# Kernel optimization log

Measured on AMD Instinct MI355X. Metric: run time of the kernel, lower is better.

## Reference

```python
import jax, jax.numpy as jnp
import numpy as np

B = 2048          # env batch
N = 32            # num_svgd_particles
D = 6             # act_dim
OBS = 17          # obs_dim
H = 256           # q1 hidden width
STEPS = 10        # num_svgd_steps
LR = 0.1          # svgd_lr
LIMIT = 1.0       # act_limit
LOG_NP1 = np.float32(np.log(N + 1.0))


def setup_inputs() -> dict:
    key = jax.random.key(0)
    ks = jax.random.split(key, 6)
    obs = jax.random.normal(ks[0], (B * N, OBS), dtype=jnp.float32)
    a = jax.random.normal(ks[1], (B * N, D), dtype=jnp.float32)
    W1 = jax.random.normal(ks[2], (OBS + D, H), dtype=jnp.float32) / np.float32(np.sqrt(OBS + D))
    b1 = jnp.zeros((H,), dtype=jnp.float32)
    W2 = jax.random.normal(ks[3], (H, H), dtype=jnp.float32) / np.float32(np.sqrt(H))
    b2 = jnp.zeros((H,), dtype=jnp.float32)
    W3 = jax.random.normal(ks[4], (H, 1), dtype=jnp.float32) / np.float32(np.sqrt(H))
    b3 = jnp.zeros((1,), dtype=jnp.float32)
    return {"obs": obs, "a": a, "W1": W1, "b1": b1, "W2": W2, "b2": b2, "W3": W3, "b3": b3}


def q1(obs, X, W1, b1, W2, b2, W3, b3):
    # standard SAC critic: Q(s, a) = MLP(concat(s, a))
    h = jax.nn.relu(jnp.concatenate([obs, X], axis=-1) @ W1 + b1)
    h = jax.nn.relu(h @ W2 + b2)
    return (h @ W3 + b3).squeeze(-1)


def rbf(X):
    # X: (B, N, D); input_2 = X.detach() in the original
    Xd = jax.lax.stop_gradient(X)
    diff = X[:, :, None, :] - Xd[:, None, :, :]          # (B, N, N, D)
    dist_sq = jnp.sum(diff * diff, axis=-1)              # (B, N, N)
    nn = N * N
    # torch.median returns the LOWER of the two middle values for even counts
    med = jnp.sort(jax.lax.stop_gradient(dist_sq).reshape(-1, nn), axis=1)[:, (nn - 1) // 2]
    h = med / (2.0 * LOG_NP1)                            # bandwidth^2 (sigma^2 = h)
    gamma = 1.0 / (1e-8 + 2.0 * h)                       # (B,)
    gamma = gamma[:, None, None]                         # (B, 1, 1)
    kappa = jnp.exp(-gamma * dist_sq)                    # (B, N, N)
    kappa_grad = -2.0 * (diff * gamma[..., None]) * kappa[..., None]  # (B, N, N, D)
    return kappa, diff, gamma, kappa_grad


def reference(obs, a, W1, b1, W2, b2, W3, b3):
    score_fn = jax.grad(lambda Xf: q1(obs, Xf, W1, b1, W2, b2, W3, b3).sum())
    logp = jnp.zeros((B, N), dtype=jnp.float32)

    for _ in range(STEPS):
        score = score_fn(a)                              # (B*N, D)
        X = a.reshape(B, N, D)
        s = score.reshape(B, N, D)
        K_XX, K_diff, K_gamma, K_grad = rbf(X)
        Kd = jax.lax.stop_gradient(K_XX)
        phi = (jnp.einsum('bij,bjd->bid', Kd, s) - K_grad.sum(axis=2)) / N  # (B, N, D)
        line_4 = (K_grad * s[:, None, :, :]).sum(-1).mean(-1)               # (B, N)
        line_5 = -2.0 * K_gamma[:, :, 0] * (
            (-K_grad * K_diff).sum(-1) - D * K_XX
        ).mean(-1)                                                          # (B, N)
        logp = logp - LR * (line_4 + line_5)
        a = jnp.clip(a + LR * phi.reshape(B * N, D), -LIMIT, LIMIT)
        a = jax.lax.stop_gradient(a)

    return a, logp
```

## Files before the change

### kernel.cpp

```cpp
#include <hip/hip_runtime.h>
#include <hip/hip_bf16.h>

#define NB 2048
#define NP 32
#define ND 6
#define NOBS 17
#define NH 256
#define NSTEPS 10
#define C_LR 0.1f
#define C_LIM 1.0f
#define C_LOGNP1 3.4965075614664802f

typedef __bf16 bf16x8 __attribute__((ext_vector_type(8)));
typedef float  f32x4  __attribute__((ext_vector_type(4)));

#define MFMA(a, b, c) __builtin_amdgcn_mfma_f32_16x16x32_bf16(a, b, c, 0, 0, 0)

static __device__ __forceinline__ unsigned short f2bf(float f) {
    union { float f; unsigned u; } c; c.f = f;
    const unsigned r = c.u + 0x7fffu + ((c.u >> 16) & 1u);
    return (unsigned short)(r >> 16);
}

static __device__ __forceinline__ int colpf(int n) {
    return ((n >> 5) << 11) + (((n >> 3) & 3) << 7) + (n & 7);
}

__global__ void prep_swizzle(const float* __restrict__ W1, const float* __restrict__ W2,
                             unsigned short* __restrict__ ws) {
    const int g = blockIdx.x * 256 + threadIdx.x;
    unsigned short v[8];
    if (g < 8192) {
        const int l = g & 63, fid = g >> 6;
        const int kt = fid >> 4, nt = fid & 15;
        const int row0 = kt * 32 + (l >> 4) * 8;
        const int col  = nt * 16 + (l & 15);
#pragma unroll
        for (int j = 0; j < 8; ++j) v[j] = f2bf(W2[(row0 + j) * NH + col]);
        ushort4* dst = (ushort4*)(ws + (size_t)g * 8);
        dst[0] = make_ushort4(v[0], v[1], v[2], v[3]);
        dst[1] = make_ushort4(v[4], v[5], v[6], v[7]);
    } else if (g < 16384) {
        const int e = g - 8192;
        const int l = e & 63, fid = e >> 6;
        const int kt = fid >> 4, nt = fid & 15;
        const int row  = nt * 16 + (l & 15);
        const int col0 = kt * 32 + (l >> 4) * 8;
#pragma unroll
        for (int j = 0; j < 8; ++j) v[j] = f2bf(W2[row * NH + col0 + j]);
        ushort4* dst = (ushort4*)(ws + 65536 + (size_t)e * 8);
        dst[0] = make_ushort4(v[0], v[1], v[2], v[3]);
        dst[1] = make_ushort4(v[4], v[5], v[6], v[7]);
    } else if (g < 16896) {
        const int e = g - 16384;
        const int l = e & 63, kt = e >> 6;
        const int n  = l & 15;
        const int k0 = kt * 32 + (l >> 4) * 8;
#pragma unroll
        for (int j = 0; j < 8; ++j)
            v[j] = (n < ND) ? f2bf(W1[(NOBS + n) * NH + k0 + j]) : (unsigned short)0;
        ushort4* dst = (ushort4*)(ws + 131072 + (size_t)e * 8);
        dst[0] = make_ushort4(v[0], v[1], v[2], v[3]);
        dst[1] = make_ushort4(v[4], v[5], v[6], v[7]);
    } else if (g < 17920) {
        const int e = g - 16896;
        const int l = e & 63, nt = e >> 6;
        const int col = nt * 16 + (l & 15);
        const int r0  = (l >> 4) * 8;
#pragma unroll
        for (int j = 0; j < 8; ++j)
            v[j] = (r0 + j < NOBS + ND) ? f2bf(W1[(r0 + j) * NH + col]) : (unsigned short)0;
        ushort4* dst = (ushort4*)(ws + 135168 + (size_t)e * 8);
        dst[0] = make_ushort4(v[0], v[1], v[2], v[3]);
        dst[1] = make_ushort4(v[4], v[5], v[6], v[7]);
    }
}

__global__ __launch_bounds__(256, 4)
void svgd_kernel(const float* __restrict__ obs, const float* __restrict__ a_in,
                 const float* __restrict__ W1, const float* __restrict__ b1,
                 const float* __restrict__ W2, const float* __restrict__ b2,
                 const float* __restrict__ W3, const unsigned short* __restrict__ ws,
                 float* __restrict__ out)
{
    __shared__ __attribute__((aligned(16))) unsigned short hA[64 * NH];
    __shared__ float Xs[2][576];
    __shared__ float sc_[576];
    __shared__ float med_s[2];

    const int t    = threadIdx.x;
    const int bb   = blockIdx.x;
    const int lane = t & 63;
    const int wid  = t >> 6;
    const int w4   = wid * 4;
    const int quad = lane >> 4;
    const int ln15 = lane & 15;
    const int qo = t >> 7, iao = (t & 127) >> 2, jgo = t & 3;

    const unsigned short* gW2f = ws;
    const unsigned short* gW2b = ws + 65536;
    const unsigned short* gW1p = ws + 131072;
    const unsigned short* gW1f = ws + 135168;

    {
        float* scr = (float*)hA;
        const float* obs_g = obs + (size_t)bb * 1088;
        for (int p = t; p < 1088; p += 256) scr[p] = obs_g[p];
        const float* a_g = a_in + (size_t)bb * 384;
        for (int p = t; p < 384; p += 256) {
            const int s = p / 6, d = p - 6 * s;
            Xs[0][s * 9 + d] = a_g[p];
        }
    }
    __syncthreads();
    bf16x8 a0[4];
    {
        const float* scr = (const float*)hA;
#pragma unroll
        for (int m = 0; m < 4; ++m) {
            const int s = m * 16 + ln15;
#pragma unroll
            for (int j = 0; j < 8; ++j) {
                const int k = quad * 8 + j;
                float v = 0.0f;
                if (k < NOBS) v = scr[s * NOBS + k];
                else if (k < NOBS + ND) v = Xs[0][s * 9 + (k - NOBS)];
                a0[m][j] = (__bf16)v;
            }
        }
    }
    __syncthreads();

    bf16x8 w1b[4]; float b1r[4], b2r[4]; unsigned short w3u[4];
#pragma unroll
    for (int q = 0; q < 4; ++q) {
        const int n = (w4 + q) * 16 + ln15;
        w1b[q] = *(const bf16x8*)(gW1f + ((w4 + q) * 64 + lane) * 8);
        b1r[q] = b1[n]; b2r[q] = b2[n]; w3u[q] = f2bf(W3[n]);
    }

    float logp_r = 0.0f;
    int cur = 0;
    const f32x4 zv = {0.f, 0.f, 0.f, 0.f};

    for (int step = 0; step < NSTEPS; ++step) {
        unsigned long long mask1 = 0ull;
#pragma unroll
        for (int p = 0; p < 2; ++p) {
            f32x4 acc0[4][2];
#pragma unroll
            for (int m = 0; m < 4; ++m)
#pragma unroll
                for (int q1 = 0; q1 < 2; ++q1)
                    acc0[m][q1] = MFMA(a0[m], w1b[2 * p + q1], zv);
#pragma unroll
            for (int q1 = 0; q1 < 2; ++q1) {
                const int q = 2 * p + q1;
                const int cp = colpf((w4 + q) * 16 + ln15);
#pragma unroll
                for (int m = 0; m < 4; ++m)
#pragma unroll
                    for (int reg = 0; reg < 4; ++reg) {
                        const float hv = acc0[m][q1][reg] + b1r[q];
                        const int idx = cp + m * 512 + (quad * 4 + reg) * 8;
                        if (hv > 0.f) {
                            mask1 |= 1ull << (q * 16 + m * 4 + reg);
                            hA[idx] = f2bf(hv);
                        } else hA[idx] = 0;
                    }
            }
        }
        __syncthreads();

        unsigned long long mask2 = 0ull;
#pragma unroll
        for (int p = 0; p < 2; ++p) {
            f32x4 acc[4][2];
#pragma unroll
            for (int m = 0; m < 4; ++m) { acc[m][0] = zv; acc[m][1] = zv; }
#pragma unroll 2
            for (int kt = 0; kt < 8; ++kt) {
                bf16x8 a[4];
#pragma unroll
                for (int m = 0; m < 4; ++m)
                    a[m] = *(const bf16x8*)&hA[(kt * 4 + m) * 512 + lane * 8];
#pragma unroll
                for (int q1 = 0; q1 < 2; ++q1) {
                    const bf16x8 bf = *(const bf16x8*)(gW2f + ((kt * 16 + w4 + 2 * p + q1) * 64 + lane) * 8);
#pragma unroll
                    for (int m = 0; m < 4; ++m) acc[m][q1] = MFMA(a[m], bf, acc[m][q1]);
                }
            }
#pragma unroll
            for (int q1 = 0; q1 < 2; ++q1)
#pragma unroll
                for (int m = 0; m < 4; ++m)
#pragma unroll
                    for (int reg = 0; reg < 4; ++reg)
                        if (acc[m][q1][reg] + b2r[2 * p + q1] > 0.f)
                            mask2 |= 1ull << ((2 * p + q1) * 16 + m * 4 + reg);
        }
        __syncthreads();
#pragma unroll
        for (int q = 0; q < 4; ++q) {
            const int cp = colpf((w4 + q) * 16 + ln15);
#pragma unroll
            for (int m = 0; m < 4; ++m)
#pragma unroll
                for (int reg = 0; reg < 4; ++reg) {
                    const int idx = cp + m * 512 + (quad * 4 + reg) * 8;
                    hA[idx] = ((mask2 >> (q * 16 + m * 4 + reg)) & 1ull)
                                  ? w3u[q] : (unsigned short)0;
                }
        }
        __syncthreads();

        unsigned dh1p[16];
        f32x4 acc2[4][2];
#pragma unroll
        for (int m = 0; m < 4; ++m) { acc2[m][0] = zv; acc2[m][1] = zv; }
#pragma unroll 2
        for (int kt = 0; kt < 8; ++kt) {
            bf16x8 a[4];
#pragma unroll
            for (int m = 0; m < 4; ++m)
                a[m] = *(const bf16x8*)&hA[(kt * 4 + m) * 512 + lane * 8];
#pragma unroll
            for (int q1 = 0; q1 < 2; ++q1) {
                const bf16x8 bf = *(const bf16x8*)(gW2b + ((kt * 16 + w4 + q1) * 64 + lane) * 8);
#pragma unroll
                for (int m = 0; m < 4; ++m) acc2[m][q1] = MFMA(a[m], bf, acc2[m][q1]);
            }
        }
#pragma unroll
        for (int q1 = 0; q1 < 2; ++q1)
#pragma unroll
            for (int m = 0; m < 4; ++m)
#pragma unroll
                for (int rp = 0; rp < 2; ++rp) {
                    const int b0 = q1 * 16 + m * 4 + rp * 2;
                    const unsigned lo = ((mask1 >> b0) & 1ull)
                        ? (unsigned)f2bf(acc2[m][q1][rp * 2]) : 0u;
                    const unsigned hi = ((mask1 >> (b0 + 1)) & 1ull)
                        ? (unsigned)f2bf(acc2[m][q1][rp * 2 + 1]) : 0u;
                    dh1p[(q1 * 4 + m) * 2 + rp] = lo | (hi << 16);
                }
#pragma unroll
        for (int m = 0; m < 4; ++m) { acc2[m][0] = zv; acc2[m][1] = zv; }
#pragma unroll 2
        for (int kt = 0; kt < 8; ++kt) {
            bf16x8 a[4];
#pragma unroll
            for (int m = 0; m < 4; ++m)
                a[m] = *(const bf16x8*)&hA[(kt * 4 + m) * 512 + lane * 8];
#pragma unroll
            for (int q1 = 0; q1 < 2; ++q1) {
                const bf16x8 bf = *(const bf16x8*)(gW2b + ((kt * 16 + w4 + 2 + q1) * 64 + lane) * 8);
#pragma unroll
                for (int m = 0; m < 4; ++m) acc2[m][q1] = MFMA(a[m], bf, acc2[m][q1]);
            }
        }
        __syncthreads();
#pragma unroll
        for (int q1 = 0; q1 < 2; ++q1) {
            const int cp = colpf((w4 + q1) * 16 + ln15);
#pragma unroll
            for (int m = 0; m < 4; ++m)
#pragma unroll
                for (int rp = 0; rp < 2; ++rp) {
                    const unsigned v = dh1p[(q1 * 4 + m) * 2 + rp];
                    const int idx = cp + m * 512 + (quad * 4 + rp * 2) * 8;
                    hA[idx]     = (unsigned short)(v & 0xffffu);
                    hA[idx + 8] = (unsigned short)(v >> 16);
                }
        }
#pragma unroll
        for (int q1 = 0; q1 < 2; ++q1) {
            const int q = 2 + q1;
            const int cp = colpf((w4 + q) * 16 + ln15);
#pragma unroll
            for (int m = 0; m < 4; ++m)
#pragma unroll
                for (int reg = 0; reg < 4; ++reg) {
                    const int idx = cp + m * 512 + (quad * 4 + reg) * 8;
                    hA[idx] = ((mask1 >> (q * 16 + m * 4 + reg)) & 1ull)
                                  ? f2bf(acc2[m][q1][reg]) : (unsigned short)0;
                }
        }
        __syncthreads();

        if (wid >= 2) {
            const int mb = (wid - 2) * 2;
            f32x4 sa[2] = {zv, zv};
#pragma unroll
            for (int kt = 0; kt < 8; ++kt) {
                const bf16x8 bw = *(const bf16x8*)(gW1p + (kt * 64 + lane) * 8);
#pragma unroll
                for (int mm = 0; mm < 2; ++mm) {
                    const bf16x8 a = *(const bf16x8*)&hA[(kt * 4 + mb + mm) * 512 + lane * 8];
                    sa[mm] = MFMA(a, bw, sa[mm]);
                }
            }
            if (ln15 < ND) {
#pragma unroll
                for (int mm = 0; mm < 2; ++mm)
#pragma unroll
                    for (int reg = 0; reg < 4; ++reg)
                        sc_[((mb + mm) * 16 + quad * 4 + reg) * 9 + ln15] = sa[mm][reg];
            }
        } else {
            const float* Xc = &Xs[cur][wid * 288];
            unsigned u[8];
#pragma unroll
            for (int r = 0; r < 8; ++r) {
                const int e = lane + 64 * r;
                if (e < 496) {
                    int i = (int)((63.0f - sqrtf(3969.0f - 8.0f * (float)e)) * 0.5f);
                    while (i * (63 - i) / 2 > e) --i;
                    while ((i + 1) * (62 - i) / 2 <= e) ++i;
                    const int j = i + 1 + (e - i * (63 - i) / 2);
                    float s = 0.f;
#pragma unroll
                    for (int d = 0; d < ND; ++d) {
                        const float df = Xc[i * 9 + d] - Xc[j * 9 + d];
                        s += df * df;
                    }
                    u[r] = __float_as_uint(s);
                } else u[r] = 0x7f800000u;
            }
            unsigned P = 0u;
            for (int bit = 30; bit >= 0; --bit) {
                const unsigned Q = P | (1u << bit);
                int c = 0;
#pragma unroll
                for (int r = 0; r < 8; ++r)
                    c += __popcll(__ballot(u[r] < Q));
                if (c <= 239) P = Q;
            }
            if (lane == 0) med_s[wid] = __uint_as_float(P);
        }
        __syncthreads();

        {
            const int nxt = cur ^ 1;
            const float gam = 1.0f / (1e-8f + med_s[qo] / C_LOGNP1);
            const float* Xc = &Xs[cur][qo * 288];
            float xi[6];
#pragma unroll
            for (int d = 0; d < ND; ++d) xi[d] = Xc[iao * 9 + d];
            float w[8] = {0, 0, 0, 0, 0, 0, 0, 0};
#pragma unroll
            for (int jj = 0; jj < 8; ++jj) {
                const int j = jgo * 8 + jj;
                float df6[6], sj6[6];
                float dsv = 0.f, dot = 0.f;
#pragma unroll
                for (int d = 0; d < ND; ++d) {
                    df6[d] = xi[d] - Xc[j * 9 + d];
                    sj6[d] = sc_[(qo * 32 + j) * 9 + d];
                    dsv += df6[d] * df6[d];
                    dot += df6[d] * sj6[d];
                }
                const float kap = __expf(-gam * dsv);
                const float tg = 2.0f * gam * kap;
#pragma unroll
                for (int d = 0; d < ND; ++d) w[d] += kap * sj6[d] + tg * df6[d];
                w[6] -= tg * dot;
                w[7] += tg * dsv - 6.0f * kap;
            }
#pragma unroll
            for (int off = 1; off < 4; off <<= 1)
#pragma unroll
                for (int c = 0; c < 8; ++c) w[c] += __shfl_xor(w[c], off);
            const int base = (qo * 32 + iao) * 9;
            {
                float x = xi[jgo] + C_LR * (w[jgo] * (1.0f / 32.0f));
                Xs[nxt][base + jgo] = fminf(fmaxf(x, -C_LIM), C_LIM);
            }
            if (jgo < 2) {
                const int d = jgo + 4;
                float x = xi[d] + C_LR * (w[d] * (1.0f / 32.0f));
                Xs[nxt][base + d] = fminf(fmaxf(x, -C_LIM), C_LIM);
            }
            if (jgo == 3)
                logp_r -= C_LR * (w[6] * (1.0f / 32.0f)
                                  - 2.0f * gam * (w[7] * (1.0f / 32.0f)));
        }
        __syncthreads();

        cur ^= 1;
        if (quad == 2) {
#pragma unroll
            for (int m = 0; m < 4; ++m) {
                const int s = m * 16 + ln15;
#pragma unroll
                for (int j = 1; j <= 6; ++j)
                    a0[m][j] = (__bf16)Xs[cur][s * 9 + (j - 1)];
            }
        }
    }

    for (int p = t; p < 384; p += 256) {
        const int s = p / 6, d = p - 6 * s;
        out[(size_t)bb * 384 + p] = Xs[cur][s * 9 + d];
    }
    if (jgo == 3) out[(size_t)NB * NP * ND + bb * 64 + qo * 32 + iao] = logp_r;
}

extern "C" void kernel_launch(void* const* d_in, const int* in_sizes, int n_in,
                              void* d_out, int out_size, void* d_ws, size_t ws_size,
                              hipStream_t stream) {
    const float* obs = (const float*)d_in[0];
    const float* a   = (const float*)d_in[1];
    const float* W1  = (const float*)d_in[2];
    const float* b1  = (const float*)d_in[3];
    const float* W2  = (const float*)d_in[4];
    const float* b2  = (const float*)d_in[5];
    const float* W3  = (const float*)d_in[6];
    unsigned short* wsu = (unsigned short*)d_ws;
    float* out = (float*)d_out;

    prep_swizzle<<<70, 256, 0, stream>>>(W1, W2, wsu);
    svgd_kernel<<<NB / 2, 256, 0, stream>>>(obs, a, W1, b1, W2, b2, W3, wsu, out);
}
```

Baseline: 558.7 us.

## Process all four column tiles per pass and compact particle shared layouts

The MLP forward and backward passes now keep all four 16-column tiles of accumulators live at once instead of splitting them into two halves. This removes the mask2 bitmask round trip, the packed dh1p spill and the extra backward GEMM pass with its barriers. W1 fragments are reloaded from global memory each step rather than held in registers. Particle and score arrays in shared memory move from padded stride 9 to dense strides 6 and 8, which shrinks LDS use but may add bank conflicts. The trade is higher accumulator register pressure, which risks spills or lower occupancy under launch_bounds(256,4).

```diff
diff --git a/kernel.cpp b/kernel.cpp
--- a/kernel.cpp
+++ b/kernel.cpp
@@ -84,8 +84,8 @@
                  float* __restrict__ out)
 {
     __shared__ __attribute__((aligned(16))) unsigned short hA[64 * NH];
-    __shared__ float Xs[2][576];
-    __shared__ float sc_[576];
+    __shared__ float Xs[2][384];
+    __shared__ float sc_[512];
     __shared__ float med_s[2];
 
     const int t    = threadIdx.x;
@@ -107,10 +107,7 @@
         const float* obs_g = obs + (size_t)bb * 1088;
         for (int p = t; p < 1088; p += 256) scr[p] = obs_g[p];
         const float* a_g = a_in + (size_t)bb * 384;
-        for (int p = t; p < 384; p += 256) {
-            const int s = p / 6, d = p - 6 * s;
-            Xs[0][s * 9 + d] = a_g[p];
-        }
+        for (int p = t; p < 384; p += 256) Xs[0][p] = a_g[p];
     }
     __syncthreads();
     bf16x8 a0[4];
@@ -124,18 +121,17 @@
                 const int k = quad * 8 + j;
                 float v = 0.0f;
                 if (k < NOBS) v = scr[s * NOBS + k];
-                else if (k < NOBS + ND) v = Xs[0][s * 9 + (k - NOBS)];
+                else if (k < NOBS + ND) v = Xs[0][s * 6 + (k - NOBS)];
                 a0[m][j] = (__bf16)v;
             }
         }
     }
     __syncthreads();
 
-    bf16x8 w1b[4]; float b1r[4], b2r[4]; unsigned short w3u[4];
+    float b1r[4], b2r[4]; unsigned short w3u[4];
 #pragma unroll
     for (int q = 0; q < 4; ++q) {
         const int n = (w4 + q) * 16 + ln15;
-        w1b[q] = *(const bf16x8*)(gW1f + ((w4 + q) * 64 + lane) * 8);
         b1r[q] = b1[n]; b2r[q] = b2[n]; w3u[q] = f2bf(W3[n]);
     }
 
@@ -145,23 +141,24 @@
 
     for (int step = 0; step < NSTEPS; ++step) {
         unsigned long long mask1 = 0ull;
-#pragma unroll
-        for (int p = 0; p < 2; ++p) {
-            f32x4 acc0[4][2];
+        {
+            bf16x8 w1B[4];
+#pragma unroll
+            for (int q = 0; q < 4; ++q)
+                w1B[q] = *(const bf16x8*)(gW1f + ((w4 + q) * 64 + lane) * 8);
+            f32x4 acc0[4][4];
 #pragma unroll
             for (int m = 0; m < 4; ++m)
 #pragma unroll
-                for (int q1 = 0; q1 < 2; ++q1)
-                    acc0[m][q1] = MFMA(a0[m], w1b[2 * p + q1], zv);
-#pragma unroll
-            for (int q1 = 0; q1 < 2; ++q1) {
-                const int q = 2 * p + q1;
+                for (int q = 0; q < 4; ++q) acc0[m][q] = MFMA(a0[m], w1B[q], zv);
+#pragma unroll
+            for (int q = 0; q < 4; ++q) {
                 const int cp = colpf((w4 + q) * 16 + ln15);
 #pragma unroll
                 for (int m = 0; m < 4; ++m)
 #pragma unroll
                     for (int reg = 0; reg < 4; ++reg) {
-                        const float hv = acc0[m][q1][reg] + b1r[q];
+                        const float hv = acc0[m][q][reg] + b1r[q];
                         const int idx = cp + m * 512 + (quad * 4 + reg) * 8;
                         if (hv > 0.f) {
                             mask1 |= 1ull << (q * 16 + m * 4 + reg);
@@ -172,12 +169,12 @@
         }
         __syncthreads();
 
-        unsigned long long mask2 = 0ull;
-#pragma unroll
-        for (int p = 0; p < 2; ++p) {
-            f32x4 acc[4][2];
-#pragma unroll
-            for (int m = 0; m < 4; ++m) { acc[m][0] = zv; acc[m][1] = zv; }
+        {
+            f32x4 acc[4][4];
+#pragma unroll
+            for (int m = 0; m < 4; ++m)
+#pragma unroll
+                for (int q = 0; q < 4; ++q) acc[m][q] = zv;
 #pragma unroll 2
             for (int kt = 0; kt < 8; ++kt) {
                 bf16x8 a[4];
@@ -185,107 +182,61 @@
                 for (int m = 0; m < 4; ++m)
                     a[m] = *(const bf16x8*)&hA[(kt * 4 + m) * 512 + lane * 8];
 #pragma unroll
-                for (int q1 = 0; q1 < 2; ++q1) {
-                    const bf16x8 bf = *(const bf16x8*)(gW2f + ((kt * 16 + w4 + 2 * p + q1) * 64 + lane) * 8);
-#pragma unroll
-                    for (int m = 0; m < 4; ++m) acc[m][q1] = MFMA(a[m], bf, acc[m][q1]);
+                for (int q = 0; q < 4; ++q) {
+                    const bf16x8 bf = *(const bf16x8*)(gW2f + ((kt * 16 + w4 + q) * 64 + lane) * 8);
+#pragma unroll
+                    for (int m = 0; m < 4; ++m) acc[m][q] = MFMA(a[m], bf, acc[m][q]);
                 }
             }
-#pragma unroll
-            for (int q1 = 0; q1 < 2; ++q1)
-#pragma unroll
-                for (int m = 0; m < 4; ++m)
-#pragma unroll
-                    for (int reg = 0; reg < 4; ++reg)
-                        if (acc[m][q1][reg] + b2r[2 * p + q1] > 0.f)
-                            mask2 |= 1ull << ((2 * p + q1) * 16 + m * 4 + reg);
-        }
-        __syncthreads();
-#pragma unroll
-        for (int q = 0; q < 4; ++q) {
-            const int cp = colpf((w4 + q) * 16 + ln15);
+            __syncthreads();
+#pragma unroll
+            for (int q = 0; q < 4; ++q) {
+                const int cp = colpf((w4 + q) * 16 + ln15);
+                const float b2v = b2r[q];
+                const unsigned short w3v = w3u[q];
+#pragma unroll
+                for (int m = 0; m < 4; ++m)
+#pragma unroll
+                    for (int reg = 0; reg < 4; ++reg) {
+                        const int idx = cp + m * 512 + (quad * 4 + reg) * 8;
+                        hA[idx] = (acc[m][q][reg] + b2v > 0.f) ? w3v : (unsigned short)0;
+                    }
+            }
+        }
+        __syncthreads();
+
+        {
+            f32x4 acc2[4][4];
 #pragma unroll
             for (int m = 0; m < 4; ++m)
 #pragma unroll
-                for (int reg = 0; reg < 4; ++reg) {
-                    const int idx = cp + m * 512 + (quad * 4 + reg) * 8;
-                    hA[idx] = ((mask2 >> (q * 16 + m * 4 + reg)) & 1ull)
-                                  ? w3u[q] : (unsigned short)0;
+                for (int q = 0; q < 4; ++q) acc2[m][q] = zv;
+#pragma unroll 2
+            for (int kt = 0; kt < 8; ++kt) {
+                bf16x8 a[4];
+#pragma unroll
+                for (int m = 0; m < 4; ++m)
+                    a[m] = *(const bf16x8*)&hA[(kt * 4 + m) * 512 + lane * 8];
+#pragma unroll
+                for (int q = 0; q < 4; ++q) {
+                    const bf16x8 bf = *(const bf16x8*)(gW2b + ((kt * 16 + w4 + q) * 64 + lane) * 8);
+#pragma unroll
+                    for (int m = 0; m < 4; ++m) acc2[m][q] = MFMA(a[m], bf, acc2[m][q]);
                 }
-        }
-        __syncthreads();
-
-        unsigned dh1p[16];
-        f32x4 acc2[4][2];
-#pragma unroll
-        for (int m = 0; m < 4; ++m) { acc2[m][0] = zv; acc2[m][1] = zv; }
-#pragma unroll 2
-        for (int kt = 0; kt < 8; ++kt) {
-            bf16x8 a[4];
-#pragma unroll
-            for (int m = 0; m < 4; ++m)
-                a[m] = *(const bf16x8*)&hA[(kt * 4 + m) * 512 + lane * 8];
-#pragma unroll
-            for (int q1 = 0; q1 < 2; ++q1) {
-                const bf16x8 bf = *(const bf16x8*)(gW2b + ((kt * 16 + w4 + q1) * 64 + lane) * 8);
-#pragma unroll
-                for (int m = 0; m < 4; ++m) acc2[m][q1] = MFMA(a[m], bf, acc2[m][q1]);
-            }
-        }
-#pragma unroll
-        for (int q1 = 0; q1 < 2; ++q1)
-#pragma unroll
-            for (int m = 0; m < 4; ++m)
-#pragma unroll
-                for (int rp = 0; rp < 2; ++rp) {
-                    const int b0 = q1 * 16 + m * 4 + rp * 2;
-                    const unsigned lo = ((mask1 >> b0) & 1ull)
-                        ? (unsigned)f2bf(acc2[m][q1][rp * 2]) : 0u;
-                    const unsigned hi = ((mask1 >> (b0 + 1)) & 1ull)
-                        ? (unsigned)f2bf(acc2[m][q1][rp * 2 + 1]) : 0u;
-                    dh1p[(q1 * 4 + m) * 2 + rp] = lo | (hi << 16);
-                }
-#pragma unroll
-        for (int m = 0; m < 4; ++m) { acc2[m][0] = zv; acc2[m][1] = zv; }
-#pragma unroll 2
-        for (int kt = 0; kt < 8; ++kt) {
-            bf16x8 a[4];
-#pragma unroll
-            for (int m = 0; m < 4; ++m)
-                a[m] = *(const bf16x8*)&hA[(kt * 4 + m) * 512 + lane * 8];
-#pragma unroll
-            for (int q1 = 0; q1 < 2; ++q1) {
-                const bf16x8 bf = *(const bf16x8*)(gW2b + ((kt * 16 + w4 + 2 + q1) * 64 + lane) * 8);
-#pragma unroll
-                for (int m = 0; m < 4; ++m) acc2[m][q1] = MFMA(a[m], bf, acc2[m][q1]);
-            }
-        }
-        __syncthreads();
-#pragma unroll
-        for (int q1 = 0; q1 < 2; ++q1) {
-            const int cp = colpf((w4 + q1) * 16 + ln15);
-#pragma unroll
-            for (int m = 0; m < 4; ++m)
-#pragma unroll
-                for (int rp = 0; rp < 2; ++rp) {
-                    const unsigned v = dh1p[(q1 * 4 + m) * 2 + rp];
-                    const int idx = cp + m * 512 + (quad * 4 + rp * 2) * 8;
-                    hA[idx]     = (unsigned short)(v & 0xffffu);
-                    hA[idx + 8] = (unsigned short)(v >> 16);
-                }
-        }
-#pragma unroll
-        for (int q1 = 0; q1 < 2; ++q1) {
-            const int q = 2 + q1;
-            const int cp = colpf((w4 + q) * 16 + ln15);
-#pragma unroll
-            for (int m = 0; m < 4; ++m)
-#pragma unroll
-                for (int reg = 0; reg < 4; ++reg) {
-                    const int idx = cp + m * 512 + (quad * 4 + reg) * 8;
-                    hA[idx] = ((mask1 >> (q * 16 + m * 4 + reg)) & 1ull)
-                                  ? f2bf(acc2[m][q1][reg]) : (unsigned short)0;
-                }
+            }
+            __syncthreads();
+#pragma unroll
+            for (int q = 0; q < 4; ++q) {
+                const int cp = colpf((w4 + q) * 16 + ln15);
+#pragma unroll
+                for (int m = 0; m < 4; ++m)
+#pragma unroll
+                    for (int reg = 0; reg < 4; ++reg) {
+                        const int idx = cp + m * 512 + (quad * 4 + reg) * 8;
+                        hA[idx] = ((mask1 >> (q * 16 + m * 4 + reg)) & 1ull)
+                                      ? f2bf(acc2[m][q][reg]) : (unsigned short)0;
+                    }
+            }
         }
         __syncthreads();
 
@@ -306,10 +257,10 @@
                 for (int mm = 0; mm < 2; ++mm)
 #pragma unroll
                     for (int reg = 0; reg < 4; ++reg)
-                        sc_[((mb + mm) * 16 + quad * 4 + reg) * 9 + ln15] = sa[mm][reg];
+                        sc_[((mb + mm) * 16 + quad * 4 + reg) * 8 + ln15] = sa[mm][reg];
             }
         } else {
-            const float* Xc = &Xs[cur][wid * 288];
+            const float* Xc = &Xs[cur][wid * 192];
             unsigned u[8];
 #pragma unroll
             for (int r = 0; r < 8; ++r) {
@@ -322,7 +273,7 @@
                     float s = 0.f;
 #pragma unroll
                     for (int d = 0; d < ND; ++d) {
-                        const float df = Xc[i * 9 + d] - Xc[j * 9 + d];
+                        const float df = Xc[i * 6 + d] - Xc[j * 6 + d];
                         s += df * df;
                     }
                     u[r] = __float_as_uint(s);
@@ -344,10 +295,10 @@
         {
             const int nxt = cur ^ 1;
             const float gam = 1.0f / (1e-8f + med_s[qo] / C_LOGNP1);
-            const float* Xc = &Xs[cur][qo * 288];
+            const float* Xc = &Xs[cur][qo * 192];
             float xi[6];
 #pragma unroll
-            for (int d = 0; d < ND; ++d) xi[d] = Xc[iao * 9 + d];
+            for (int d = 0; d < ND; ++d) xi[d] = Xc[iao * 6 + d];
             float w[8] = {0, 0, 0, 0, 0, 0, 0, 0};
 #pragma unroll
             for (int jj = 0; jj < 8; ++jj) {
@@ -356,8 +307,8 @@
                 float dsv = 0.f, dot = 0.f;
 #pragma unroll
                 for (int d = 0; d < ND; ++d) {
-                    df6[d] = xi[d] - Xc[j * 9 + d];
-                    sj6[d] = sc_[(qo * 32 + j) * 9 + d];
+                    df6[d] = xi[d] - Xc[j * 6 + d];
+                    sj6[d] = sc_[(qo * 32 + j) * 8 + d];
                     dsv += df6[d] * df6[d];
                     dot += df6[d] * sj6[d];
                 }
@@ -372,7 +323,7 @@
             for (int off = 1; off < 4; off <<= 1)
 #pragma unroll
                 for (int c = 0; c < 8; ++c) w[c] += __shfl_xor(w[c], off);
-            const int base = (qo * 32 + iao) * 9;
+            const int base = (qo * 32 + iao) * 6;
             {
                 float x = xi[jgo] + C_LR * (w[jgo] * (1.0f / 32.0f));
                 Xs[nxt][base + jgo] = fminf(fmaxf(x, -C_LIM), C_LIM);
@@ -395,15 +346,12 @@
                 const int s = m * 16 + ln15;
 #pragma unroll
                 for (int j = 1; j <= 6; ++j)
-                    a0[m][j] = (__bf16)Xs[cur][s * 9 + (j - 1)];
-            }
-        }
-    }
-
-    for (int p = t; p < 384; p += 256) {
-        const int s = p / 6, d = p - 6 * s;
-        out[(size_t)bb * 384 + p] = Xs[cur][s * 9 + d];
-    }
+                    a0[m][j] = (__bf16)Xs[cur][s * 6 + (j - 1)];
+            }
+        }
+    }
+
+    for (int p = t; p < 384; p += 256) out[(size_t)bb * 384 + p] = Xs[cur][p];
     if (jgo == 3) out[(size_t)NB * NP * ND + bb * 64 + qo * 32 + iao] = logp_r;
 }
 
```

After: 488.5 us. -12.6%, faster.
